# Optimization experiments

Measured on AMD Instinct MI355X. Metric: run time of the kernel, lower is better.

## Reference

```python
import jax, jax.numpy as jnp
import numpy as np

NUM_HEADS = 16
HEAD_DIM = 64  # hidden_size 1024 / 16 heads


def setup_inputs() -> dict:
    key = jax.random.key(0)
    ks = jax.random.split(key, 5)
    B, S, D = 4, 2048, 1024
    std = 0.02
    return {
        "hidden_states": jax.random.normal(ks[0], (B, S, D), jnp.float32),
        "attention_mask": jnp.zeros((B, 1, 1, S), jnp.float32),
        "Wq": jax.random.normal(ks[1], (D, D), jnp.float32) * std,
        "bq": jnp.zeros((D,), jnp.float32),
        "Wk": jax.random.normal(ks[2], (D, D), jnp.float32) * std,
        "bk": jnp.zeros((D,), jnp.float32),
        "Wv": jax.random.normal(ks[3], (D, D), jnp.float32) * std,
        "bv": jnp.zeros((D,), jnp.float32),
    }


def _split_heads(x):
    # [B, S, H*dh] -> [B, H, S, dh]
    B, S, _ = x.shape
    return x.reshape(B, S, NUM_HEADS, HEAD_DIM).transpose(0, 2, 1, 3)


def reference(hidden_states, attention_mask, Wq, bq, Wk, bk, Wv, bv):
    q = _split_heads(hidden_states @ Wq + bq)  # [B,H,S,dh]
    k = _split_heads(hidden_states @ Wk + bk)
    v = _split_heads(hidden_states @ Wv + bv)
    scale = 1.0 / jnp.sqrt(jnp.asarray(HEAD_DIM, q.dtype))
    scores = jnp.einsum("bhqd,bhkd->bhqk", q, k) * scale
    scores = scores + attention_mask.astype(scores.dtype)
    probs = jax.nn.softmax(scores, axis=-1)  # dropout prob = 0 -> identity
    ctx = jnp.einsum("bhqk,bhkd->bhqd", probs, v)
    B, H, S, dh = ctx.shape
    return ctx.transpose(0, 2, 1, 3).reshape(B, S, H * dh)
```

## Files before the change

kernel.cpp:

```cpp
#include <hip/hip_runtime.h>
#include <stdint.h>

typedef unsigned short u16;
typedef __attribute__((ext_vector_type(4))) float f32x4;
typedef __attribute__((ext_vector_type(8))) short bf16x8;
typedef __attribute__((ext_vector_type(4))) int i32x4;

#define LOG2E 1.4426950408889634f

__device__ inline u16 f2b(float x) {
  union { float f; uint32_t u; } t; t.f = x;
  uint32_t r = t.u + 0x7FFFu + ((t.u >> 16) & 1u);
  return (u16)(r >> 16);
}

__device__ inline int cvtpk(float a, float b) {
  int r;
  asm("v_cvt_pk_bf16_f32 %0, %1, %2" : "=v"(r) : "v"(a), "v"(b));
  return r;
}

__device__ inline float exp2a(float x) {
  float r;
  asm("v_exp_f32 %0, %1" : "=v"(r) : "v"(x));
  return r;
}

typedef const __attribute__((address_space(1))) void* gas_t;
typedef __attribute__((address_space(3))) void* las_t;
__device__ inline void gld16(const void* g, void* l) {
  __builtin_amdgcn_global_load_lds((gas_t)g, (las_t)l, 16, 0, 0);
}

__global__ void cvt_hs_k(const float* __restrict__ in, u16* __restrict__ outp, int n) {
  int i = (blockIdx.x * 256 + threadIdx.x) * 4;
  if (i >= n) return;
  float4 v = *(const float4*)(in + i);
  ushort4 o = { f2b(v.x), f2b(v.y), f2b(v.z), f2b(v.w) };
  *(ushort4*)(outp + i) = o;
}

__global__ void twk(const float* __restrict__ Wq, const float* __restrict__ Wk,
                    const float* __restrict__ Wv, u16* __restrict__ Wt) {
  __shared__ float tile[64][65];
  const float* W = (blockIdx.z == 0) ? Wq : ((blockIdx.z == 1) ? Wk : Wv);
  int n0 = blockIdx.x * 64, k0 = blockIdx.y * 64;
  int tid = threadIdx.x;
#pragma unroll 4
  for (int i = 0; i < 16; ++i) {
    int idx = i * 256 + tid; int r = idx >> 6, c = idx & 63;
    tile[r][c] = W[(k0 + r) * 1024 + n0 + c];
  }
  __syncthreads();
  u16* dst = Wt + blockIdx.z * 1048576;
#pragma unroll 4
  for (int i = 0; i < 16; ++i) {
    int idx = i * 256 + tid; int r = idx >> 6, c = idx & 63;
    dst[(n0 + r) * 1024 + k0 + c] = f2b(tile[c][r]);
  }
}

__global__ __launch_bounds__(256) void qkv_gemm_k(
    const u16* __restrict__ hsb, const u16* __restrict__ wt,
    const float* __restrict__ bq, const float* __restrict__ bk, const float* __restrict__ bv,
    u16* __restrict__ Qo, u16* __restrict__ Ko, u16* __restrict__ Vto) {
  __shared__ u16 lh[2][128 * 64];
  __shared__ u16 lw[2][128 * 64];
  const int tid = threadIdx.x;
  const int w = tid >> 6, l = tid & 63, g = l >> 4, lm = l & 15;
  const int wm = w >> 1, wn = w & 1;

  int lin = blockIdx.y * 24 + blockIdx.x;
  lin = (lin & 7) * 192 + (lin >> 3);
  const int bx = lin % 24, by = lin / 24;
  const int nbase = bx << 7;
  const int wi = nbase >> 10;
  const int nloc0 = nbase & 1023;
  const int mbase = by << 7;
  const u16* hsg = hsb + (size_t)mbase * 1024;
  const u16* wg  = wt + (size_t)wi * 1048576 + (size_t)nloc0 * 1024;

  f32x4 acc[4][4];
#pragma unroll
  for (int i = 0; i < 4; ++i)
#pragma unroll
    for (int j = 0; j < 4; ++j)
#pragma unroll
      for (int r = 0; r < 4; ++r) acc[i][j][r] = 0.f;

  const int key = lm & 7;
  const int fb0 = lm * 64 + ((g ^ key) << 3);
  const int fb1 = lm * 64 + (((g + 4) ^ key) << 3);

#pragma unroll
  for (int p = 0; p < 4; ++p) {
    int idx = p * 256 + tid;
    int r = idx >> 3, c = idx & 7;
    int sc = (c ^ (r & 7)) << 3;
    gld16(hsg + (size_t)r * 1024 + sc, &lh[0][idx * 8]);
    gld16(wg + (size_t)r * 1024 + sc, &lw[0][idx * 8]);
  }

  for (int t = 0; t < 16; ++t) {
    const int cur = t & 1;
    if (t < 15) {
      const int kb = (t + 1) << 6;
#pragma unroll
      for (int p = 0; p < 4; ++p) {
        int idx = p * 256 + tid;
        int r = idx >> 3, c = idx & 7;
        int sc = (c ^ (r & 7)) << 3;
        gld16(hsg + (size_t)r * 1024 + kb + sc, &lh[cur ^ 1][idx * 8]);
        gld16(wg + (size_t)r * 1024 + kb + sc, &lw[cur ^ 1][idx * 8]);
      }
      asm volatile("s_waitcnt vmcnt(8)" ::: "memory");
    } else {
      asm volatile("s_waitcnt vmcnt(0)" ::: "memory");
    }
    __builtin_amdgcn_s_barrier();

    const u16* LH = lh[cur] + wm * 64 * 64;
    const u16* LW = lw[cur] + wn * 64 * 64;
    bf16x8 fh[4][2], fw[4][2];
#pragma unroll
    for (int i = 0; i < 4; ++i) {
      fh[i][0] = *(const bf16x8*)(LH + i * 1024 + fb0);
      fh[i][1] = *(const bf16x8*)(LH + i * 1024 + fb1);
      fw[i][0] = *(const bf16x8*)(LW + i * 1024 + fb0);
      fw[i][1] = *(const bf16x8*)(LW + i * 1024 + fb1);
    }
    __builtin_amdgcn_s_setprio(1);
    if (wi < 2) {
#pragma unroll
      for (int ks = 0; ks < 2; ++ks)
#pragma unroll
        for (int mi = 0; mi < 4; ++mi)
#pragma unroll
          for (int ni = 0; ni < 4; ++ni)
            acc[mi][ni] = __builtin_amdgcn_mfma_f32_16x16x32_bf16(fw[ni][ks], fh[mi][ks], acc[mi][ni], 0, 0, 0);
    } else {
#pragma unroll
      for (int ks = 0; ks < 2; ++ks)
#pragma unroll
        for (int mi = 0; mi < 4; ++mi)
#pragma unroll
          for (int ni = 0; ni < 4; ++ni)
            acc[mi][ni] = __builtin_amdgcn_mfma_f32_16x16x32_bf16(fh[mi][ks], fw[ni][ks], acc[mi][ni], 0, 0, 0);
    }
    __builtin_amdgcn_s_setprio(0);
    __builtin_amdgcn_s_barrier();
  }

  if (wi < 2) {
    u16* O = (wi == 0) ? Qo : Ko;
    const float* bias = (wi == 0) ? bq : bk;
#pragma unroll
    for (int ni = 0; ni < 4; ++ni) {
      int nl = nloc0 + wn * 64 + ni * 16 + g * 4;
      f32x4 b4 = *(const f32x4*)(bias + nl);
      int d = nl & 63, h = nl >> 6;
#pragma unroll
      for (int mi = 0; mi < 4; ++mi) {
        int m = mbase + wm * 64 + mi * 16 + lm;
        int bb = m >> 11, s = m & 2047;
        f32x4 v = acc[mi][ni];
        int2 o = { cvtpk(v[0] + b4[0], v[1] + b4[1]), cvtpk(v[2] + b4[2], v[3] + b4[3]) };
        *(int2*)(O + ((size_t)(bb * 16 + h) * 2048 + s) * 64 + d) = o;
      }
    }
  } else {
#pragma unroll
    for (int ni = 0; ni < 4; ++ni) {
      int nl = nloc0 + wn * 64 + ni * 16 + lm;
      float bsc = bv[nl];
      int d = nl & 63, h = nl >> 6;
#pragma unroll
      for (int mi = 0; mi < 4; ++mi) {
        int m = mbase + wm * 64 + mi * 16 + g * 4;
        int bb = m >> 11, s = m & 2047;
        int cp = (s & ~31) | (((s >> 2) & 3) << 3) | (((s >> 4) & 1) << 2);
        f32x4 v = acc[mi][ni];
        int2 o = { cvtpk(v[0] + bsc, v[1] + bsc), cvtpk(v[2] + bsc, v[3] + bsc) };
        *(int2*)(Vto + ((size_t)(bb * 16 + h) * 64 + d) * 2048 + cp) = o;
      }
    }
  }
}

__global__ __launch_bounds__(512) void attn_k(
    const u16* __restrict__ Qg, const u16* __restrict__ Kg, const u16* __restrict__ Vtg,
    const float* __restrict__ maskg, float* __restrict__ outp) {
  __shared__ u16 kts[2][64 * 64];
  __shared__ u16 vts[2][64 * 64];
  __shared__ float ml[2048];
  const int tid = threadIdx.x;
  const int w = tid >> 6, l = tid & 63, g = l >> 4, lm = l & 15;

  int bid = blockIdx.y * 16 + blockIdx.x;
  bid = (bid & 7) * 128 + (bid >> 3);
  const int bx = bid & 15, bh = bid >> 4;
  const int b = bh >> 4, h = bh & 15;
  const int q0 = bx * 128 + w * 16;
  const u16* Qb = Qg + ((size_t)bh * 2048 + q0) * 64;
  const u16* Kb = Kg + (size_t)bh * 2048 * 64;
  const u16* Vb = Vtg + (size_t)bh * 64 * 2048;
  const float* mb = maskg + b * 2048;

  bf16x8 qf0 = *(const bf16x8*)(Qb + lm * 64 + g * 8);
  bf16x8 qf1 = *(const bf16x8*)(Qb + lm * 64 + 32 + g * 8);

  f32x4 ctx[4];
#pragma unroll
  for (int dt = 0; dt < 4; ++dt)
#pragma unroll
    for (int r = 0; r < 4; ++r) ctx[dt][r] = 0.f;
  float lrun = 0.f;
  const float QS = 0.125f * LOG2E;
  const f32x4 zf = { 0.f, 0.f, 0.f, 0.f };

  const int key = lm & 7;
  const int fb0 = lm * 64 + ((g ^ key) << 3);
  const int fb1 = lm * 64 + (((g + 4) ^ key) << 3);
  const float* mlb = ml + g * 4;

  const int rk = tid >> 3, ck = tid & 7;
  {
    f32x4 mv = *(const f32x4*)(mb + tid * 4);
    *(f32x4*)(ml + tid * 4) = mv * LOG2E - 8.0f;
  }
  gld16(Kb + (size_t)rk * 64 + ((ck ^ (rk & 7)) << 3), &kts[0][tid * 8]);
  gld16(Vb + (size_t)rk * 2048 + ((ck ^ (rk & 7)) << 3), &vts[0][tid * 8]);
  __syncthreads();

  for (int t = 0; t < 32; ++t) {
    const int kv = t << 6, cur = t & 1;
    if (t < 31) {
      const int kv2 = kv + 64;
      gld16(Kb + (size_t)(kv2 + rk) * 64 + ((ck ^ (rk & 7)) << 3), &kts[cur ^ 1][tid * 8]);
      gld16(Vb + (size_t)rk * 2048 + kv2 + ((ck ^ (rk & 7)) << 3), &vts[cur ^ 1][tid * 8]);
      asm volatile("s_waitcnt vmcnt(2)" ::: "memory");
    } else {
      asm volatile("s_waitcnt vmcnt(0)" ::: "memory");
    }
    __builtin_amdgcn_s_barrier();

    const u16* kt = kts[cur];
    const u16* vt = vts[cur];

    f32x4 st[4];
    __builtin_amdgcn_s_setprio(1);
#pragma unroll
    for (int t8 = 0; t8 < 4; ++t8) {
      bf16x8 kf = *(const bf16x8*)(kt + t8 * 1024 + fb0);
      st[t8] = __builtin_amdgcn_mfma_f32_16x16x32_bf16(kf, qf0, zf, 0, 0, 0);
    }
#pragma unroll
    for (int t8 = 0; t8 < 4; ++t8) {
      bf16x8 kf = *(const bf16x8*)(kt + t8 * 1024 + fb1);
      st[t8] = __builtin_amdgcn_mfma_f32_16x16x32_bf16(kf, qf1, st[t8], 0, 0, 0);
    }
    __builtin_amdgcn_s_setprio(0);

    int pt[4][2];
#pragma unroll
    for (int t8 = 0; t8 < 4; ++t8) {
      f32x4 mv = *(const f32x4*)(mlb + kv + t8 * 16);
      float p0 = exp2a(fmaf(st[t8][0], QS, mv[0]));
      float p1 = exp2a(fmaf(st[t8][1], QS, mv[1]));
      float p2 = exp2a(fmaf(st[t8][2], QS, mv[2]));
      float p3 = exp2a(fmaf(st[t8][3], QS, mv[3]));
      lrun += (p0 + p1) + (p2 + p3);
      pt[t8][0] = cvtpk(p0, p1);
      pt[t8][1] = cvtpk(p2, p3);
    }

    __builtin_amdgcn_s_setprio(1);
#pragma unroll
    for (int tp = 0; tp < 2; ++tp) {
      i32x4 pbi = { pt[2 * tp][0], pt[2 * tp][1], pt[2 * tp + 1][0], pt[2 * tp + 1][1] };
      bf16x8 pb = __builtin_bit_cast(bf16x8, pbi);
      const int fb = tp ? fb1 : fb0;
#pragma unroll
      for (int dt = 0; dt < 4; ++dt) {
        bf16x8 va = *(const bf16x8*)(vt + dt * 1024 + fb);
        ctx[dt] = __builtin_amdgcn_mfma_f32_16x16x32_bf16(va, pb, ctx[dt], 0, 0, 0);
      }
    }
    __builtin_amdgcn_s_setprio(0);
    __builtin_amdgcn_s_barrier();
  }

  lrun += __shfl_xor(lrun, 16);
  lrun += __shfl_xor(lrun, 32);
  float inv = 1.f / lrun;
  int sq = q0 + lm;
  float* ob = outp + ((size_t)(b * 2048 + sq)) * 1024 + h * 64;
#pragma unroll
  for (int dt = 0; dt < 4; ++dt) {
    f32x4 o;
#pragma unroll
    for (int r = 0; r < 4; ++r) o[r] = ctx[dt][r] * inv;
    *(f32x4*)(ob + dt * 16 + g * 4) = o;
  }
}

extern "C" void kernel_launch(void* const* d_in, const int* in_sizes, int n_in,
                              void* d_out, int out_size, void* d_ws, size_t ws_size,
                              hipStream_t stream) {
  const float* hs   = (const float*)d_in[0];
  const float* mask = (const float*)d_in[1];
  const float* Wq   = (const float*)d_in[2];
  const float* bq   = (const float*)d_in[3];
  const float* Wk   = (const float*)d_in[4];
  const float* bk   = (const float*)d_in[5];
  const float* Wv   = (const float*)d_in[6];
  const float* bv   = (const float*)d_in[7];
  float* out = (float*)d_out;

  char* ws = (char*)d_ws;
  u16* hsb = (u16*)(ws);
  u16* wt  = (u16*)(ws + (16u << 20));
  u16* Qb  = (u16*)(ws + (24u << 20));
  u16* Kb  = (u16*)(ws + (40u << 20));
  u16* Vtb = (u16*)(ws + (56u << 20));

  cvt_hs_k<<<dim3(8192), dim3(256), 0, stream>>>(hs, hsb, 8388608);
  twk<<<dim3(16, 16, 3), dim3(256), 0, stream>>>(Wq, Wk, Wv, wt);
  qkv_gemm_k<<<dim3(24, 64), dim3(256), 0, stream>>>(hsb, wt, bq, bk, bv, Qb, Kb, Vtb);
  attn_k<<<dim3(16, 64), dim3(512), 0, stream>>>(Qb, Kb, Vtb, mask, out);
}
```

Measured before the change: 260.5 us.

## Software-pipeline QK and PV in attention and halve GEMM K-tile

The attention loop is restructured so the QK^T MFMAs for the next KV tile are issued before the softmax and PV of the current tile, with K prefetched two tiles ahead and V one tile ahead. This is meant to overlap exp/convert VALU work with matrix-core work. The QKV GEMM separately drops its K-step from 64 to 32, halving LDS per stage (likely to raise occupancy) with a new swizzle layout, at the cost of twice as many barriers per output tile.

Result: slower. 280.0 us (+7.5%).

```diff
diff --git a/kernel.cpp b/kernel.cpp
--- a/kernel.cpp
+++ b/kernel.cpp
@@ -64,8 +64,8 @@
     const u16* __restrict__ hsb, const u16* __restrict__ wt,
     const float* __restrict__ bq, const float* __restrict__ bk, const float* __restrict__ bv,
     u16* __restrict__ Qo, u16* __restrict__ Ko, u16* __restrict__ Vto) {
-  __shared__ u16 lh[2][128 * 64];
-  __shared__ u16 lw[2][128 * 64];
+  __shared__ u16 lh[2][128 * 32];
+  __shared__ u16 lw[2][128 * 32];
   const int tid = threadIdx.x;
   const int w = tid >> 6, l = tid & 63, g = l >> 4, lm = l & 15;
   const int wm = w >> 1, wn = w & 1;
@@ -88,64 +88,54 @@
 #pragma unroll
       for (int r = 0; r < 4; ++r) acc[i][j][r] = 0.f;
 
-  const int key = lm & 7;
-  const int fb0 = lm * 64 + ((g ^ key) << 3);
-  const int fb1 = lm * 64 + (((g + 4) ^ key) << 3);
-
-#pragma unroll
-  for (int p = 0; p < 4; ++p) {
-    int idx = p * 256 + tid;
-    int r = idx >> 3, c = idx & 7;
-    int sc = (c ^ (r & 7)) << 3;
-    gld16(hsg + (size_t)r * 1024 + sc, &lh[0][idx * 8]);
-    gld16(wg + (size_t)r * 1024 + sc, &lw[0][idx * 8]);
-  }
-
-  for (int t = 0; t < 16; ++t) {
+  const int i0 = tid, i1 = tid + 256;
+  const int r0 = ((i0 >> 3) << 1) + ((i0 >> 2) & 1), c0 = ((i0 & 3) ^ ((i0 >> 3) & 3)) << 3;
+  const int r1 = ((i1 >> 3) << 1) + ((i1 >> 2) & 1), c1 = ((i1 & 3) ^ ((i1 >> 3) & 3)) << 3;
+
+  const int so = (((lm & 1) << 2) + (g ^ ((lm >> 1) & 3))) << 3;
+  const int fbm = (wm * 32 + (lm >> 1)) * 64 + so;
+  const int fbn = (wn * 32 + (lm >> 1)) * 64 + so;
+
+  gld16(hsg + (size_t)r0 * 1024 + c0, &lh[0][i0 * 8]);
+  gld16(hsg + (size_t)r1 * 1024 + c1, &lh[0][i1 * 8]);
+  gld16(wg + (size_t)r0 * 1024 + c0, &lw[0][i0 * 8]);
+  gld16(wg + (size_t)r1 * 1024 + c1, &lw[0][i1 * 8]);
+
+  for (int t = 0; t < 32; ++t) {
     const int cur = t & 1;
-    if (t < 15) {
-      const int kb = (t + 1) << 6;
-#pragma unroll
-      for (int p = 0; p < 4; ++p) {
-        int idx = p * 256 + tid;
-        int r = idx >> 3, c = idx & 7;
-        int sc = (c ^ (r & 7)) << 3;
-        gld16(hsg + (size_t)r * 1024 + kb + sc, &lh[cur ^ 1][idx * 8]);
-        gld16(wg + (size_t)r * 1024 + kb + sc, &lw[cur ^ 1][idx * 8]);
-      }
-      asm volatile("s_waitcnt vmcnt(8)" ::: "memory");
+    if (t < 31) {
+      const int kb = (t + 1) << 5;
+      gld16(hsg + (size_t)r0 * 1024 + kb + c0, &lh[cur ^ 1][i0 * 8]);
+      gld16(hsg + (size_t)r1 * 1024 + kb + c1, &lh[cur ^ 1][i1 * 8]);
+      gld16(wg + (size_t)r0 * 1024 + kb + c0, &lw[cur ^ 1][i0 * 8]);
+      gld16(wg + (size_t)r1 * 1024 + kb + c1, &lw[cur ^ 1][i1 * 8]);
+      asm volatile("s_waitcnt vmcnt(4)" ::: "memory");
     } else {
       asm volatile("s_waitcnt vmcnt(0)" ::: "memory");
     }
     __builtin_amdgcn_s_barrier();
 
-    const u16* LH = lh[cur] + wm * 64 * 64;
-    const u16* LW = lw[cur] + wn * 64 * 64;
-    bf16x8 fh[4][2], fw[4][2];
+    const u16* LH = lh[cur];
+    const u16* LW = lw[cur];
+    bf16x8 fh[4], fw[4];
 #pragma unroll
     for (int i = 0; i < 4; ++i) {
-      fh[i][0] = *(const bf16x8*)(LH + i * 1024 + fb0);
-      fh[i][1] = *(const bf16x8*)(LH + i * 1024 + fb1);
-      fw[i][0] = *(const bf16x8*)(LW + i * 1024 + fb0);
-      fw[i][1] = *(const bf16x8*)(LW + i * 1024 + fb1);
+      fh[i] = *(const bf16x8*)(LH + fbm + i * 512);
+      fw[i] = *(const bf16x8*)(LW + fbn + i * 512);
     }
     __builtin_amdgcn_s_setprio(1);
     if (wi < 2) {
 #pragma unroll
-      for (int ks = 0; ks < 2; ++ks)
-#pragma unroll
-        for (int mi = 0; mi < 4; ++mi)
-#pragma unroll
-          for (int ni = 0; ni < 4; ++ni)
-            acc[mi][ni] = __builtin_amdgcn_mfma_f32_16x16x32_bf16(fw[ni][ks], fh[mi][ks], acc[mi][ni], 0, 0, 0);
+      for (int mi = 0; mi < 4; ++mi)
+#pragma unroll
+        for (int ni = 0; ni < 4; ++ni)
+          acc[mi][ni] = __builtin_amdgcn_mfma_f32_16x16x32_bf16(fw[ni], fh[mi], acc[mi][ni], 0, 0, 0);
     } else {
 #pragma unroll
-      for (int ks = 0; ks < 2; ++ks)
-#pragma unroll
-        for (int mi = 0; mi < 4; ++mi)
-#pragma unroll
-          for (int ni = 0; ni < 4; ++ni)
-            acc[mi][ni] = __builtin_amdgcn_mfma_f32_16x16x32_bf16(fh[mi][ks], fw[ni][ks], acc[mi][ni], 0, 0, 0);
+      for (int mi = 0; mi < 4; ++mi)
+#pragma unroll
+        for (int ni = 0; ni < 4; ++ni)
+          acc[mi][ni] = __builtin_amdgcn_mfma_f32_16x16x32_bf16(fh[mi], fw[ni], acc[mi][ni], 0, 0, 0);
     }
     __builtin_amdgcn_s_setprio(0);
     __builtin_amdgcn_s_barrier();
@@ -224,70 +214,100 @@
   const float* mlb = ml + g * 4;
 
   const int rk = tid >> 3, ck = tid & 7;
+  const int swz = (ck ^ (rk & 7)) << 3;
+
+#define QK_BLOCK(KT, ST)                                                        \
+  do {                                                                          \
+    __builtin_amdgcn_s_setprio(1);                                              \
+    _Pragma("unroll") for (int t8 = 0; t8 < 4; ++t8) {                          \
+      bf16x8 kf = *(const bf16x8*)((KT) + t8 * 1024 + fb0);                     \
+      ST[t8] = __builtin_amdgcn_mfma_f32_16x16x32_bf16(kf, qf0, zf, 0, 0, 0);   \
+    }                                                                           \
+    _Pragma("unroll") for (int t8 = 0; t8 < 4; ++t8) {                          \
+      bf16x8 kf = *(const bf16x8*)((KT) + t8 * 1024 + fb1);                     \
+      ST[t8] = __builtin_amdgcn_mfma_f32_16x16x32_bf16(kf, qf1, ST[t8], 0, 0, 0);\
+    }                                                                           \
+    __builtin_amdgcn_s_setprio(0);                                              \
+  } while (0)
+
+#define SM_BLOCK(ST, KV)                                                        \
+  do {                                                                          \
+    _Pragma("unroll") for (int t8 = 0; t8 < 4; ++t8) {                          \
+      f32x4 mv = *(const f32x4*)(mlb + (KV) + t8 * 16);                         \
+      float p0 = exp2a(fmaf(ST[t8][0], QS, mv[0]));                             \
+      float p1 = exp2a(fmaf(ST[t8][1], QS, mv[1]));                             \
+      float p2 = exp2a(fmaf(ST[t8][2], QS, mv[2]));                             \
+      float p3 = exp2a(fmaf(ST[t8][3], QS, mv[3]));                             \
+      lrun += (p0 + p1) + (p2 + p3);                                            \
+      pt[t8][0] = cvtpk(p0, p1);                                                \
+      pt[t8][1] = cvtpk(p2, p3);                                                \
+    }                                                                           \
+  } while (0)
+
+#define PV_BLOCK(VT)                                                            \
+  do {                                                                          \
+    __builtin_amdgcn_s_setprio(1);                                              \
+    _Pragma("unroll") for (int tp = 0; tp < 2; ++tp) {                          \
+      i32x4 pbi = { pt[2 * tp][0], pt[2 * tp][1],                               \
+                    pt[2 * tp + 1][0], pt[2 * tp + 1][1] };                     \
+      bf16x8 pb = __builtin_bit_cast(bf16x8, pbi);                              \
+      const int fb = tp ? fb1 : fb0;                                            \
+      _Pragma("unroll") for (int dt = 0; dt < 4; ++dt) {                        \
+        bf16x8 va = *(const bf16x8*)((VT) + dt * 1024 + fb);                    \
+        ctx[dt] = __builtin_amdgcn_mfma_f32_16x16x32_bf16(va, pb, ctx[dt], 0, 0, 0);\
+      }                                                                         \
+    }                                                                           \
+    __builtin_amdgcn_s_setprio(0);                                              \
+  } while (0)
+
   {
     f32x4 mv = *(const f32x4*)(mb + tid * 4);
     *(f32x4*)(ml + tid * 4) = mv * LOG2E - 8.0f;
   }
-  gld16(Kb + (size_t)rk * 64 + ((ck ^ (rk & 7)) << 3), &kts[0][tid * 8]);
-  gld16(Vb + (size_t)rk * 2048 + ((ck ^ (rk & 7)) << 3), &vts[0][tid * 8]);
+  gld16(Kb + (size_t)rk * 64 + swz, &kts[0][tid * 8]);
+  gld16(Vb + (size_t)rk * 2048 + swz, &vts[0][tid * 8]);
+  gld16(Kb + (size_t)(64 + rk) * 64 + swz, &kts[1][tid * 8]);
   __syncthreads();
 
-  for (int t = 0; t < 32; ++t) {
-    const int kv = t << 6, cur = t & 1;
-    if (t < 31) {
-      const int kv2 = kv + 64;
-      gld16(Kb + (size_t)(kv2 + rk) * 64 + ((ck ^ (rk & 7)) << 3), &kts[cur ^ 1][tid * 8]);
-      gld16(Vb + (size_t)rk * 2048 + kv2 + ((ck ^ (rk & 7)) << 3), &vts[cur ^ 1][tid * 8]);
-      asm volatile("s_waitcnt vmcnt(2)" ::: "memory");
-    } else {
-      asm volatile("s_waitcnt vmcnt(0)" ::: "memory");
-    }
-    __builtin_amdgcn_s_barrier();
-
-    const u16* kt = kts[cur];
-    const u16* vt = vts[cur];
-
-    f32x4 st[4];
-    __builtin_amdgcn_s_setprio(1);
-#pragma unroll
-    for (int t8 = 0; t8 < 4; ++t8) {
-      bf16x8 kf = *(const bf16x8*)(kt + t8 * 1024 + fb0);
-      st[t8] = __builtin_amdgcn_mfma_f32_16x16x32_bf16(kf, qf0, zf, 0, 0, 0);
-    }
-#pragma unroll
-    for (int t8 = 0; t8 < 4; ++t8) {
-      bf16x8 kf = *(const bf16x8*)(kt + t8 * 1024 + fb1);
-      st[t8] = __builtin_amdgcn_mfma_f32_16x16x32_bf16(kf, qf1, st[t8], 0, 0, 0);
-    }
-    __builtin_amdgcn_s_setprio(0);
-
-    int pt[4][2];
-#pragma unroll
-    for (int t8 = 0; t8 < 4; ++t8) {
-      f32x4 mv = *(const f32x4*)(mlb + kv + t8 * 16);
-      float p0 = exp2a(fmaf(st[t8][0], QS, mv[0]));
-      float p1 = exp2a(fmaf(st[t8][1], QS, mv[1]));
-      float p2 = exp2a(fmaf(st[t8][2], QS, mv[2]));
-      float p3 = exp2a(fmaf(st[t8][3], QS, mv[3]));
-      lrun += (p0 + p1) + (p2 + p3);
-      pt[t8][0] = cvtpk(p0, p1);
-      pt[t8][1] = cvtpk(p2, p3);
-    }
-
-    __builtin_amdgcn_s_setprio(1);
-#pragma unroll
-    for (int tp = 0; tp < 2; ++tp) {
-      i32x4 pbi = { pt[2 * tp][0], pt[2 * tp][1], pt[2 * tp + 1][0], pt[2 * tp + 1][1] };
-      bf16x8 pb = __builtin_bit_cast(bf16x8, pbi);
-      const int fb = tp ? fb1 : fb0;
-#pragma unroll
-      for (int dt = 0; dt < 4; ++dt) {
-        bf16x8 va = *(const bf16x8*)(vt + dt * 1024 + fb);
-        ctx[dt] = __builtin_amdgcn_mfma_f32_16x16x32_bf16(va, pb, ctx[dt], 0, 0, 0);
-      }
-    }
-    __builtin_amdgcn_s_setprio(0);
-    __builtin_amdgcn_s_barrier();
+  f32x4 stp[4];
+  QK_BLOCK(kts[0], stp);
+  __builtin_amdgcn_s_barrier();
+
+  int pt[4][2];
+  for (int t = 0; t < 30; ++t) {
+    const int cur = t & 1;
+    gld16(Vb + (size_t)rk * 2048 + ((t + 1) << 6) + swz, &vts[cur ^ 1][tid * 8]);
+    gld16(Kb + (size_t)(((t + 2) << 6) + rk) * 64 + swz, &kts[cur][tid * 8]);
+    asm volatile("s_waitcnt vmcnt(2)" ::: "memory");
+    __builtin_amdgcn_s_barrier();
+
+    f32x4 stn[4];
+    QK_BLOCK(kts[cur ^ 1], stn);
+    __builtin_amdgcn_sched_barrier(0);
+    SM_BLOCK(stp, t << 6);
+    PV_BLOCK(vts[cur]);
+#pragma unroll
+    for (int t8 = 0; t8 < 4; ++t8) stp[t8] = stn[t8];
+    __builtin_amdgcn_s_barrier();
+  }
+  {
+    gld16(Vb + (size_t)rk * 2048 + (31 << 6) + swz, &vts[1][tid * 8]);
+    asm volatile("s_waitcnt vmcnt(1)" ::: "memory");
+    __builtin_amdgcn_s_barrier();
+    f32x4 stn[4];
+    QK_BLOCK(kts[1], stn);
+    __builtin_amdgcn_sched_barrier(0);
+    SM_BLOCK(stp, 30 << 6);
+    PV_BLOCK(vts[0]);
+#pragma unroll
+    for (int t8 = 0; t8 < 4; ++t8) stp[t8] = stn[t8];
+    __builtin_amdgcn_s_barrier();
+  }
+  {
+    asm volatile("s_waitcnt vmcnt(0)" ::: "memory");
+    __builtin_amdgcn_s_barrier();
+    SM_BLOCK(stp, 31 << 6);
+    PV_BLOCK(vts[1]);
   }
 
   lrun += __shfl_xor(lrun, 16);
@@ -302,6 +322,9 @@
     for (int r = 0; r < 4; ++r) o[r] = ctx[dt][r] * inv;
     *(f32x4*)(ob + dt * 16 + g * 4) = o;
   }
+#undef QK_BLOCK
+#undef SM_BLOCK
+#undef PV_BLOCK
 }
 
 extern "C" void kernel_launch(void* const* d_in, const int* in_sizes, int n_in,
```
